# Performance work log

Measured on AMD Instinct MI355X. Metric: run time of the kernel, lower is better.

## Reference

```python
import jax, jax.numpy as jnp
import numpy as np

PI = 3.141592653589793
TAU = 2.0      # tau for both rpe_lif (spikingjelly default 2.0) and act_conv (params['tau'])
V_TH = 1.0     # spikingjelly LIFNode default v_threshold
EPS = 1e-5     # LayerNorm / BatchNorm eps


@jax.custom_vjp
def atan_spike(x):
    # Heaviside forward, ATan surrogate backward (spikingjelly surrogate.ATan, alpha=2)
    return (x >= 0.0).astype(x.dtype)

def _atan_fwd(x):
    return atan_spike(x), x

def _atan_bwd(x, g):
    # (alpha/2) / (1 + ((pi/2)*alpha*x)^2) with alpha=2 -> 1/(1+(pi*x)^2)
    return (g / (1.0 + (PI * x) ** 2),)

atan_spike.defvjp(_atan_fwd, _atan_bwd)


def lif(x_seq, tau=TAU):
    """Multi-step LIF: decay_input=True, v_reset=0, hard reset, detach_reset.
    x_seq: [T, ...]; returns spikes [T, ...]."""
    def step(v, x):
        v = v + (x - v) / tau                      # neuronal charge
        s = atan_spike(v - V_TH)                   # fire
        v = v * (1.0 - jax.lax.stop_gradient(s))   # detached hard reset to 0
        return v, s
    _, spikes = jax.lax.scan(step, jnp.zeros_like(x_seq[0]), x_seq)
    return spikes


def setup_inputs() -> dict:
    key = jax.random.key(0)
    ks = jax.random.split(key, 8)
    B, L, D, T = 256, 50, 128, 4
    n_items, n_h, n_v = 100001, 8, 4
    emb = jax.random.normal(ks[0], (n_items, D), jnp.float32) * 0.5
    emb = emb.at[0].set(0.0)  # padding_idx=0
    return {
        "item_seq": jax.random.randint(ks[1], (B, L), 0, n_items, jnp.int32),
        "emb_table": emb,
        "ln_gamma": jnp.ones((D,), jnp.float32),
        "ln_beta": jnp.zeros((D,), jnp.float32),
        "conv_v_w": jax.random.normal(ks[2], (n_v, L), jnp.float32) * float(1.0 / np.sqrt(L)),
        # per-length kernels stored padded: kernel for length k=i+1 is conv_h_w[i, :, :k, :]
        "conv_h_w": jax.random.normal(ks[3], (L, n_h, L, D), jnp.float32) * 0.02,
        "bn_gamma": jnp.ones((L, n_h), jnp.float32),
        "bn_beta": jnp.zeros((L, n_h), jnp.float32),
        "fc_h_w": jax.random.normal(ks[4], (D, n_h * L), jnp.float32) * 0.05,
        "fc_h_b": jnp.zeros((D,), jnp.float32),
        "fc_v_w": jax.random.normal(ks[5], (D, n_v * D), jnp.float32) * 0.04,
        "fc_v_b": jnp.zeros((D,), jnp.float32),
        "T": 4,
    }


def reference(item_seq, emb_table, ln_gamma, ln_beta, conv_v_w, conv_h_w,
              bn_gamma, bn_beta, fc_h_w, fc_h_b, fc_v_w, fc_v_b, T):
    B, L = item_seq.shape
    D = emb_table.shape[1]
    n_h = conv_h_w.shape[1]
    n_v = conv_v_w.shape[0]

    # embedding + LayerNorm
    emb = emb_table[item_seq]                                   # [B,L,D]
    mu = emb.mean(-1, keepdims=True)
    var = emb.var(-1, keepdims=True)
    x = (emb - mu) / jnp.sqrt(var + EPS) * ln_gamma + ln_beta   # [B,L,D]

    # repeat over T and spike (rpe_lif)
    s = lif(jnp.broadcast_to(x, (T, B, L, D)))                  # binary spikes [T,B,L,D]

    # vertical conv: kernel (L,1), no bias -> collapses seq axis
    out_v = jnp.einsum('tbld,cl->tbcd', s, conv_v_w).reshape(T, B, n_v * D)

    # horizontal multi-scale convs + BN(train stats) + LIF + global max pool
    s2 = s.reshape(T * B, 1, L, D)
    pools = []
    for i in range(L):
        k = i + 1
        w = conv_h_w[i, :, :k, :][:, None]                      # [n_h,1,k,D]
        y = jax.lax.conv_general_dilated(
            s2, w, (1, 1), 'VALID',
            dimension_numbers=('NCHW', 'OIHW', 'NCHW'))[:, :, :, 0]  # [TB,n_h,L-k+1]
        m = y.mean(axis=(0, 2))                                  # BN over (T*B, spatial)
        v = y.var(axis=(0, 2))
        y = (y - m[:, None]) * (bn_gamma[i][:, None] / jnp.sqrt(v[:, None] + EPS)) + bn_beta[i][:, None]
        y = lif(y.reshape(T, B, n_h, L - k + 1))                 # [T,B,n_h,L-k+1]
        pools.append(y.max(axis=-1))                             # [T,B,n_h]
    out_h = jnp.concatenate(pools, axis=-1)                      # [T,B,n_h*L]

    out_h = (out_h @ fc_h_w.T + fc_h_b).mean(0)                  # [B,D]
    out_v = out_v.mean(0) @ fc_v_w.T + fc_v_b                    # [B,D]
    return out_h + out_v
```

## Files before the change

### kernel.cpp

```cpp
#include <hip/hip_runtime.h>

#define B_ 256
#define L_ 50
#define D_ 128
#define T_ 4
#define NH 8
#define NV 4
#define TB_ (T_*B_)
#define EPSF 1e-5f

typedef _Float16 h8 __attribute__((ext_vector_type(8)));
typedef float f4 __attribute__((ext_vector_type(4)));

typedef __attribute__((address_space(1))) const unsigned int gas_u32;
typedef __attribute__((address_space(3))) unsigned int las_u32;
#define GLOAD_LDS16(gp, lp) __builtin_amdgcn_global_load_lds((gas_u32*)(gp), (las_u32*)(lp), 16, 0, 0)

__device__ __forceinline__ float waveSum(float v) {
    #pragma unroll
    for (int o = 32; o > 0; o >>= 1) v += __shfl_down(v, o, 64);
    return v;
}

__device__ __forceinline__ size_t yoff(int i) {
    return (size_t)8192 * (size_t)(50 * i - (i * (i - 1)) / 2);
}

__global__ __launch_bounds__(256) void k0_wsplit(
        const float* __restrict__ w, _Float16* __restrict__ whl) {
    int dk = blockIdx.x, i = blockIdx.y;
    int t = threadIdx.x;
    int c = t >> 4, gd = t & 15;
    int h = c & 7;
    bool live = (i < 50) && (dk <= i);
    const float* src = w + (((size_t)i * NH + h) * L_ + dk) * D_ + gd * 8;
    h8 o;
    #pragma unroll
    for (int e = 0; e < 8; ++e) {
        float wv = live ? src[e] : 0.f;
        _Float16 hi = (_Float16)wv;
        o[e] = (c < 8) ? hi : (_Float16)((wv - (float)hi) * 1024.f);
    }
    *(h8*)(whl + (((size_t)i * 50 + dk) * 16 + c) * 128 + ((gd ^ c) & 15) * 8) = o;
}

__global__ __launch_bounds__(128) void k1_embed_ln_lif(
        const int* __restrict__ item, const float* __restrict__ tab,
        const float* __restrict__ g, const float* __restrict__ be,
        _Float16* __restrict__ s16, float* __restrict__ smean) {
    int bid = blockIdx.x;
    int b = bid / L_, l = bid % L_;
    int d = threadIdx.x;
    int wid = d >> 6, lane = d & 63;
    __shared__ float red[2];
    int it = item[b * L_ + l];
    float e = tab[(size_t)it * D_ + d];
    float sm_ = waveSum(e);
    if (lane == 0) red[wid] = sm_;
    __syncthreads();
    float mu = (red[0] + red[1]) * (1.f / 128.f);
    __syncthreads();
    float df = e - mu;
    float s2 = waveSum(df * df);
    if (lane == 0) red[wid] = s2;
    __syncthreads();
    float var = (red[0] + red[1]) * (1.f / 128.f);
    float x = df / sqrtf(var + EPSF) * g[d] + be[d];
    float v = 0.f, acc = 0.f;
    int pos = (((d >> 3) ^ l) & 15) * 8 + (d & 7);
    #pragma unroll
    for (int t = 0; t < T_; ++t) {
        v += (x - v) * 0.5f;
        float sp = (v >= 1.f) ? 1.f : 0.f;
        v *= (1.f - sp);
        s16[((size_t)(t * B_ + b) * L_ + l) * D_ + pos] = (_Float16)sp;
        acc += sp;
    }
    smean[((size_t)b * L_ + l) * D_ + d] = acc * 0.25f;
}

template<int MTG>
__global__ __launch_bounds__(512, 2) void k2u(
        const _Float16* __restrict__ s16, const _Float16* __restrict__ whl,
        float* __restrict__ y, int gbase) {
    extern __shared__ __align__(16) char lds[];
    char* Bslot = lds + 102400;
    const int NM = 2 * MTG;
    const int tbo = blockIdx.x;
    const int grp = gbase + blockIdx.y;
    const int i0 = grp * 4;
    const int kmax = i0 + 4;
    const int tid = threadIdx.x;
    const int wave = tid >> 6, lane = tid & 63;
    const int p = wave >> 1;
    const int dh = wave & 1;
    const int c_ = lane & 15, g = lane >> 4;

    {
        const float4* src = (const float4*)(s16 + (size_t)tbo * 8 * (L_ * D_));
        float4* dst = (float4*)lds;
        for (int idx = tid; idx < 6400; idx += 512) dst[idx] = src[idx];
    }
    const char* bsrc = (const char*)whl + (size_t)i0 * 50 * 4096;
    const int o0 = tid * 16, o1 = 8192 + tid * 16;
    const int sc0 = o0 >> 12, r0 = o0 & 4095;
    const int sc1 = o1 >> 12, r1 = o1 & 4095;
    const char* g0p = bsrc + (size_t)sc0 * (50 * 4096) + r0;
    const char* g1p = bsrc + (size_t)sc1 * (50 * 4096) + r1;

    float4 n0 = *(const float4*)(g0p);
    float4 n1 = *(const float4*)(g1p);
    __syncthreads();
    *(float4*)(Bslot + o0) = n0;
    *(float4*)(Bslot + o1) = n1;
    __syncthreads();

    f4 acc[4][NM];
    #pragma unroll
    for (int sc = 0; sc < 4; ++sc)
        #pragma unroll
        for (int m = 0; m < NM; ++m) { f4 z = {0.f, 0.f, 0.f, 0.f}; acc[sc][m] = z; }

    for (int dk = 0; dk < kmax; ++dk) {
        const bool more = (dk + 1 < kmax);
        float4 m0, m1;
        if (more) {
            m0 = *(const float4*)(g0p + (size_t)(dk + 1) * 4096);
            m1 = *(const float4*)(g1p + (size_t)(dk + 1) * 4096);
        }
        __builtin_amdgcn_sched_barrier(0);
        #pragma unroll
        for (int dci = 0; dci < 2; ++dci) {
            const int dc = dh * 2 + dci;
            h8 bf[4];
            #pragma unroll
            for (int sc = 0; sc < 4; ++sc)
                bf[sc] = *(const h8*)(Bslot + sc * 4096 + c_ * 256 +
                                      ((((dc << 2) + g) ^ c_) & 15) * 16);
            #pragma unroll
            for (int m = 0; m < NM; ++m) {
                const int tbL = p * 2 + (m >= MTG ? 1 : 0);
                const int jt = (m >= MTG) ? m - MTG : m;
                int l = jt * 16 + c_ + dk; if (l > 49) l = 49;
                h8 a = *(const h8*)(lds + tbL * 12800 + l * 256 +
                                    ((((dc << 2) + g) ^ l) & 15) * 16);
                #pragma unroll
                for (int sc = 0; sc < 4; ++sc)
                    acc[sc][m] = __builtin_amdgcn_mfma_f32_16x16x32_f16(a, bf[sc], acc[sc][m], 0, 0, 0);
            }
        }
        __syncthreads();
        if (more) {
            *(float4*)(Bslot + o0) = m0;
            *(float4*)(Bslot + o1) = m1;
        }
        __syncthreads();
    }

    const int STR = 2 * NM * 4 + 4;
    float* mbuf = (float*)lds;
    #pragma unroll
    for (int half = 0; half < 2; ++half) {
        __syncthreads();
        if (dh == 1) {
            float* wp = mbuf + (size_t)(p * 64 + lane) * STR;
            #pragma unroll
            for (int sc = 0; sc < 2; ++sc)
                #pragma unroll
                for (int m = 0; m < NM; ++m)
                    *(f4*)(wp + (sc * NM + m) * 4) = acc[2 * half + sc][m];
        }
        __syncthreads();
        if (dh == 0) {
            const float* rp = mbuf + (size_t)(p * 64 + lane) * STR;
            #pragma unroll
            for (int sc = 0; sc < 2; ++sc)
                #pragma unroll
                for (int m = 0; m < NM; ++m)
                    acc[2 * half + sc][m] += *(const f4*)(rp + (sc * NM + m) * 4);
        }
    }

    if (dh == 0) {
        const bool hiLane = (c_ < 8);
        const int h = c_ & 7;
        #pragma unroll
        for (int sc = 0; sc < 4; ++sc) {
            const int i = i0 + sc;
            const int J = 50 - i;
            #pragma unroll
            for (int m = 0; m < NM; ++m) {
                const int tbL = p * 2 + (m >= MTG ? 1 : 0);
                const int jt = (m >= MTG) ? m - MTG : m;
                const int tb = tbo * 8 + tbL;
                size_t yb = yoff(i) + ((size_t)tb * NH + h) * J;
                #pragma unroll
                for (int r = 0; r < 4; ++r) {
                    float lo = __shfl_xor(acc[sc][m][r], 8, 64);
                    int j = jt * 16 + g * 4 + r;
                    if (hiLane && j < J) y[yb + j] = acc[sc][m][r] + lo * (1.f / 1024.f);
                }
            }
        }
    }
}

__global__ __launch_bounds__(256, 1) void k2c(
        const _Float16* __restrict__ s16, const _Float16* __restrict__ whl,
        float* __restrict__ y) {
    extern __shared__ __align__(16) char lds[];
    char* bring = lds + 102400;
    const int tbo = blockIdx.x;
    const int i0 = 36 + blockIdx.y * 4;
    const int kmax = (i0 + 4 <= 50) ? (i0 + 4) : 50;
    const int tid = threadIdx.x;
    const int wave = tid >> 6, lane = tid & 63;
    const int tq = wave & 1, sg = wave >> 1;
    const int c_ = lane & 15, g = lane >> 4;

    {
        const float4* src = (const float4*)(s16 + (size_t)tbo * 8 * (L_ * D_));
        float4* dst = (float4*)lds;
        for (int idx = tid; idx < 6400; idx += 256) dst[idx] = src[idx];
    }
    const char* bsrc = (const char*)(whl + ((size_t)(i0 + wave) * 50) * 2048);
    {
        #pragma unroll
        for (int s = 0; s < 2; ++s) {
            const char* gp = bsrc + (size_t)s * 4096 + lane * 16;
            char* lp = bring + s * 16384 + wave * 4096 + lane * 16;
            #pragma unroll
            for (int q = 0; q < 4; ++q)
                GLOAD_LDS16(gp + q * 1024, lp + q * 1024);
        }
    }
    asm volatile("s_waitcnt lgkmcnt(0)" ::: "memory");
    __builtin_amdgcn_s_barrier();
    __builtin_amdgcn_sched_barrier(0);

    f4 acc[2][4];
    #pragma unroll
    for (int s = 0; s < 2; ++s)
        #pragma unroll
        for (int t = 0; t < 4; ++t) { f4 z = {0.f, 0.f, 0.f, 0.f}; acc[s][t] = z; }

    const char* Aq = lds + (tq * 4) * 12800;
    int boff[4];
    #pragma unroll
    for (int dc = 0; dc < 4; ++dc)
        boff[dc] = c_ * 256 + ((((dc << 2) + g) ^ c_) & 15) * 16;

    int rdpos = 0, wrpos = 32768;
    for (int dk = 0; dk < kmax; ++dk) {
        if (dk + 1 < kmax) asm volatile("s_waitcnt vmcnt(4)" ::: "memory");
        else               asm volatile("s_waitcnt vmcnt(0)" ::: "memory");
        __builtin_amdgcn_s_barrier();
        __builtin_amdgcn_sched_barrier(0);
        if (dk + 2 < kmax) {
            const char* gp = bsrc + (size_t)(dk + 2) * 4096 + lane * 16;
            char* lp = bring + wrpos + wave * 4096 + lane * 16;
            #pragma unroll
            for (int q = 0; q < 4; ++q)
                GLOAD_LDS16(gp + q * 1024, lp + q * 1024);
        }
        const char* Bs = bring + rdpos + sg * 8192;
        #pragma unroll
        for (int dc = 0; dc < 4; ++dc) {
            h8 b0 = *(const h8*)(Bs + boff[dc]);
            h8 b1 = *(const h8*)(Bs + 4096 + boff[dc]);
            int l = c_ + dk; if (l > 49) l = 49;
            int aoff = l * 256 + ((((dc << 2) + g) ^ l) & 15) * 16;
            #pragma unroll
            for (int tbL = 0; tbL < 4; ++tbL) {
                h8 a = *(const h8*)(Aq + tbL * 12800 + aoff);
                acc[0][tbL] = __builtin_amdgcn_mfma_f32_16x16x32_f16(a, b0, acc[0][tbL], 0, 0, 0);
                acc[1][tbL] = __builtin_amdgcn_mfma_f32_16x16x32_f16(a, b1, acc[1][tbL], 0, 0, 0);
            }
        }
        rdpos += 16384; if (rdpos == 49152) rdpos = 0;
        wrpos += 16384; if (wrpos == 49152) wrpos = 0;
    }
    const bool hiLane = (c_ < 8);
    const int h = c_ & 7;
    #pragma unroll
    for (int s = 0; s < 2; ++s) {
        const int i = i0 + sg * 2 + s;
        const int J = 50 - i;
        if (J <= 0) continue;
        #pragma unroll
        for (int tbL = 0; tbL < 4; ++tbL) {
            const int tb = tbo * 8 + tq * 4 + tbL;
            size_t yb = yoff(i) + ((size_t)tb * NH + h) * J;
            #pragma unroll
            for (int r = 0; r < 4; ++r) {
                float lo = __shfl_xor(acc[s][tbL][r], 8, 64);
                int j = g * 4 + r;
                if (hiLane && j < J) y[yb + j] = acc[s][tbL][r] + lo * (1.f / 1024.f);
            }
        }
    }
}

__global__ __launch_bounds__(256) void k3_partial(
        const float* __restrict__ y, float* __restrict__ psum) {
    int ih = blockIdx.x, ck = blockIdx.y;
    int i = ih >> 3, h = ih & 7;
    int J = 50 - i;
    size_t yb = yoff(i);
    int tid = threadIdx.x;
    int grp = tid >> 5, sub = tid & 31;
    float sm = 0.f, ss = 0.f;
    for (int tb = ck * 128 + grp; tb < (ck + 1) * 128; tb += 8) {
        const float* row = y + yb + ((size_t)tb * NH + h) * J;
        for (int j = sub; j < J; j += 32) { float v = row[j]; sm += v; ss += v * v; }
    }
    __shared__ float r1[4], r2[4];
    float a = waveSum(sm), b = waveSum(ss);
    int wid = tid >> 6, lane = tid & 63;
    if (lane == 0) { r1[wid] = a; r2[wid] = b; }
    __syncthreads();
    if (tid == 0) {
        psum[((size_t)ih * 8 + ck) * 2]     = r1[0] + r1[1] + r1[2] + r1[3];
        psum[((size_t)ih * 8 + ck) * 2 + 1] = r2[0] + r2[1] + r2[2] + r2[3];
    }
}

__global__ __launch_bounds__(256) void k3_final(
        const float* __restrict__ psum, const float* __restrict__ bng,
        float* __restrict__ statm, float* __restrict__ stats_) {
    int ih = blockIdx.x * 256 + threadIdx.x;
    if (ih >= 400) return;
    float S = 0.f, Q = 0.f;
    for (int ck = 0; ck < 8; ++ck) {
        S += psum[((size_t)ih * 8 + ck) * 2];
        Q += psum[((size_t)ih * 8 + ck) * 2 + 1];
    }
    int i = ih >> 3;
    float cnt = 1024.f * (float)(50 - i);
    float m = S / cnt;
    float var = Q / cnt - m * m; if (var < 0.f) var = 0.f;
    statm[ih] = m;
    stats_[ih] = bng[ih] / sqrtf(var + EPSF);
}

__global__ __launch_bounds__(512) void k4_bn_lif_pool(
        const float* __restrict__ y, const float* __restrict__ statm,
        const float* __restrict__ stats_, const float* __restrict__ bnb,
        float* __restrict__ ps) {
    int b = blockIdx.x, i = blockIdx.y, J = L_ - i;
    int h = threadIdx.x >> 6, lane = threadIdx.x & 63;
    int ih = i * NH + h;
    float m = statm[ih], sc = stats_[ih], bb = bnb[ih];
    size_t yb = yoff(i);
    bool valid = lane < J;
    float v = 0.f; int cnt = 0;
    #pragma unroll
    for (int t = 0; t < T_; ++t) {
        int tb = t * B_ + b;
        float yn;
        if (valid) {
            float raw = y[yb + ((size_t)tb * NH + h) * J + lane];
            yn = (raw - m) * sc + bb;
        } else yn = -1e30f;
        v += (yn - v) * 0.5f;
        bool sp = (v >= 1.f);
        if (sp) v = 0.f;
        if (__any(sp)) cnt++;
    }
    if (lane == 0) ps[(size_t)b * 400 + ih] = (float)cnt;
}

__global__ __launch_bounds__(128) void k5_final(
        const float* __restrict__ smean, const float* __restrict__ ps,
        const float* __restrict__ convv, const float* __restrict__ fchw,
        const float* __restrict__ fchb, const float* __restrict__ fcvw,
        const float* __restrict__ fcvb, float* __restrict__ out) {
    __shared__ float sm_l[L_ * D_];
    __shared__ float vm[NV * D_];
    __shared__ float ps_l[400];
    int b = blockIdx.x, tid = threadIdx.x;
    for (int idx = tid; idx < L_ * D_; idx += 128) sm_l[idx] = smean[(size_t)b * (L_ * D_) + idx];
    for (int idx = tid; idx < 400; idx += 128) ps_l[idx] = ps[(size_t)b * 400 + idx];
    __syncthreads();
    int d = tid;
    #pragma unroll
    for (int c = 0; c < NV; ++c) {
        float a = 0.f;
        for (int l = 0; l < L_; ++l) a += convv[c * L_ + l] * sm_l[l * D_ + d];
        vm[c * D_ + d] = a;
    }
    __syncthreads();
    float acc = fchb[d] + fcvb[d];
    float ah = 0.f;
    for (int ih = 0; ih < 400; ++ih) ah += ps_l[ih] * fchw[d * 400 + ih];
    acc += ah * 0.25f;
    float av = 0.f;
    for (int cd = 0; cd < NV * D_; ++cd) av += vm[cd] * fcvw[d * (NV * D_) + cd];
    acc += av;
    out[(size_t)b * D_ + d] = acc;
}

extern "C" void kernel_launch(void* const* d_in, const int* in_sizes, int n_in,
                              void* d_out, int out_size, void* d_ws, size_t ws_size,
                              hipStream_t stream) {
    const int*   item  = (const int*)d_in[0];
    const float* tab   = (const float*)d_in[1];
    const float* lng   = (const float*)d_in[2];
    const float* lnb   = (const float*)d_in[3];
    const float* convv = (const float*)d_in[4];
    const float* convh = (const float*)d_in[5];
    const float* bng   = (const float*)d_in[6];
    const float* bnb   = (const float*)d_in[7];
    const float* fchw  = (const float*)d_in[8];
    const float* fchb  = (const float*)d_in[9];
    const float* fcvw  = (const float*)d_in[10];
    const float* fcvb  = (const float*)d_in[11];
    float* out = (float*)d_out;

    char* ws = (char*)d_ws;
    _Float16* s16  = (_Float16*)(ws);
    float* smean   = (float*)(ws + 13107200LL);
    float* y       = (float*)(ws + 19660800LL);
    _Float16* whl  = (_Float16*)(ws + 61440000LL);
    float* statm   = (float*)(ws + 72089600LL);
    float* stats_  = (float*)(ws + 72091200LL);
    float* ps      = (float*)(ws + 72092800LL);
    float* psum    = (float*)(ws + 72502400LL);

    hipFuncSetAttribute(reinterpret_cast<const void*>(&k2u<4>),
        hipFuncAttributeMaxDynamicSharedMemorySize, 118784);
    hipFuncSetAttribute(reinterpret_cast<const void*>(&k2u<3>),
        hipFuncAttributeMaxDynamicSharedMemorySize, 118784);
    hipFuncSetAttribute(reinterpret_cast<const void*>(&k2u<2>),
        hipFuncAttributeMaxDynamicSharedMemorySize, 118784);
    hipFuncSetAttribute(reinterpret_cast<const void*>(&k2c),
        hipFuncAttributeMaxDynamicSharedMemorySize, 151552);

    k0_wsplit<<<dim3(50, 52), 256, 0, stream>>>(convh, whl);
    k1_embed_ln_lif<<<B_ * L_, 128, 0, stream>>>(item, tab, lng, lnb, s16, smean);
    k2u<4><<<dim3(128, 1), 512, 118784, stream>>>(s16, whl, y, 0);
    k2u<3><<<dim3(128, 4), 512, 118784, stream>>>(s16, whl, y, 1);
    k2u<2><<<dim3(128, 4), 512, 118784, stream>>>(s16, whl, y, 5);
    k2c<<<dim3(128, 4), 256, 151552, stream>>>(s16, whl, y);
    k3_partial<<<dim3(400, 8), 256, 0, stream>>>(y, psum);
    k3_final<<<dim3(2, 1), 256, 0, stream>>>(psum, bng, statm, stats_);
    k4_bn_lif_pool<<<dim3(B_, L_), 512, 0, stream>>>(y, statm, stats_, bnb, ps);
    k5_final<<<B_, 128, 0, stream>>>(smean, ps, convv, fchw, fchb, fcvw, fcvb, out);
}
```

Measured before the change: 290.6 us.

## Split tail conv kernel across D-chunks with eight waves and LDS reduction

Rewrites the tail multi-scale conv kernel (scales 36-49) to use 512 threads, where each wave owns one D-chunk and all four scales and the partial accumulators are reduced through LDS at the end. The old three-slot async global-to-LDS ring for the weights becomes a register-prefetched single LDS slot with two barriers per step. This lowers LDS to 118784 bytes and gives more waves per block, so the tail kernel gets more parallelism and latency hiding. The costs are extra barriers, a reduction pass, and serialized weight staging.

```diff
diff --git a/kernel.cpp b/kernel.cpp
--- a/kernel.cpp
+++ b/kernel.cpp
@@ -205,97 +205,109 @@
     }
 }
 
-__global__ __launch_bounds__(256, 1) void k2c(
+__global__ __launch_bounds__(512, 2) void k2t(
         const _Float16* __restrict__ s16, const _Float16* __restrict__ whl,
         float* __restrict__ y) {
     extern __shared__ __align__(16) char lds[];
-    char* bring = lds + 102400;
+    char* Bslot = lds + 102400;
     const int tbo = blockIdx.x;
     const int i0 = 36 + blockIdx.y * 4;
     const int kmax = (i0 + 4 <= 50) ? (i0 + 4) : 50;
     const int tid = threadIdx.x;
     const int wave = tid >> 6, lane = tid & 63;
-    const int tq = wave & 1, sg = wave >> 1;
+    const int tq = wave >> 2;
+    const int dc = wave & 3;
     const int c_ = lane & 15, g = lane >> 4;
 
     {
         const float4* src = (const float4*)(s16 + (size_t)tbo * 8 * (L_ * D_));
         float4* dst = (float4*)lds;
-        for (int idx = tid; idx < 6400; idx += 256) dst[idx] = src[idx];
-    }
-    const char* bsrc = (const char*)(whl + ((size_t)(i0 + wave) * 50) * 2048);
-    {
-        #pragma unroll
-        for (int s = 0; s < 2; ++s) {
-            const char* gp = bsrc + (size_t)s * 4096 + lane * 16;
-            char* lp = bring + s * 16384 + wave * 4096 + lane * 16;
-            #pragma unroll
-            for (int q = 0; q < 4; ++q)
-                GLOAD_LDS16(gp + q * 1024, lp + q * 1024);
-        }
-    }
-    asm volatile("s_waitcnt lgkmcnt(0)" ::: "memory");
-    __builtin_amdgcn_s_barrier();
-    __builtin_amdgcn_sched_barrier(0);
-
-    f4 acc[2][4];
-    #pragma unroll
-    for (int s = 0; s < 2; ++s)
-        #pragma unroll
-        for (int t = 0; t < 4; ++t) { f4 z = {0.f, 0.f, 0.f, 0.f}; acc[s][t] = z; }
-
-    const char* Aq = lds + (tq * 4) * 12800;
-    int boff[4];
-    #pragma unroll
-    for (int dc = 0; dc < 4; ++dc)
-        boff[dc] = c_ * 256 + ((((dc << 2) + g) ^ c_) & 15) * 16;
-
-    int rdpos = 0, wrpos = 32768;
+        for (int idx = tid; idx < 6400; idx += 512) dst[idx] = src[idx];
+    }
+    const char* bsrc = (const char*)whl + (size_t)i0 * 50 * 4096;
+    const int o0 = tid * 16, o1 = 8192 + tid * 16;
+    const char* g0p = bsrc + (size_t)(o0 >> 12) * (50 * 4096) + (o0 & 4095);
+    const char* g1p = bsrc + (size_t)(o1 >> 12) * (50 * 4096) + (o1 & 4095);
+    float4 n0 = *(const float4*)(g0p);
+    float4 n1 = *(const float4*)(g1p);
+    __syncthreads();
+    *(float4*)(Bslot + o0) = n0;
+    *(float4*)(Bslot + o1) = n1;
+    __syncthreads();
+
+    f4 acc[4][4];
+    #pragma unroll
+    for (int sc = 0; sc < 4; ++sc)
+        #pragma unroll
+        for (int tt = 0; tt < 4; ++tt) { f4 z = {0.f, 0.f, 0.f, 0.f}; acc[sc][tt] = z; }
+
+    const int boffc = c_ * 256 + ((((dc << 2) + g) ^ c_) & 15) * 16;
     for (int dk = 0; dk < kmax; ++dk) {
-        if (dk + 1 < kmax) asm volatile("s_waitcnt vmcnt(4)" ::: "memory");
-        else               asm volatile("s_waitcnt vmcnt(0)" ::: "memory");
-        __builtin_amdgcn_s_barrier();
+        const bool more = (dk + 1 < kmax);
+        float4 m0, m1;
+        if (more) {
+            m0 = *(const float4*)(g0p + (size_t)(dk + 1) * 4096);
+            m1 = *(const float4*)(g1p + (size_t)(dk + 1) * 4096);
+        }
         __builtin_amdgcn_sched_barrier(0);
-        if (dk + 2 < kmax) {
-            const char* gp = bsrc + (size_t)(dk + 2) * 4096 + lane * 16;
-            char* lp = bring + wrpos + wave * 4096 + lane * 16;
-            #pragma unroll
-            for (int q = 0; q < 4; ++q)
-                GLOAD_LDS16(gp + q * 1024, lp + q * 1024);
-        }
-        const char* Bs = bring + rdpos + sg * 8192;
-        #pragma unroll
-        for (int dc = 0; dc < 4; ++dc) {
-            h8 b0 = *(const h8*)(Bs + boff[dc]);
-            h8 b1 = *(const h8*)(Bs + 4096 + boff[dc]);
-            int l = c_ + dk; if (l > 49) l = 49;
-            int aoff = l * 256 + ((((dc << 2) + g) ^ l) & 15) * 16;
-            #pragma unroll
-            for (int tbL = 0; tbL < 4; ++tbL) {
-                h8 a = *(const h8*)(Aq + tbL * 12800 + aoff);
-                acc[0][tbL] = __builtin_amdgcn_mfma_f32_16x16x32_f16(a, b0, acc[0][tbL], 0, 0, 0);
-                acc[1][tbL] = __builtin_amdgcn_mfma_f32_16x16x32_f16(a, b1, acc[1][tbL], 0, 0, 0);
-            }
-        }
-        rdpos += 16384; if (rdpos == 49152) rdpos = 0;
-        wrpos += 16384; if (wrpos == 49152) wrpos = 0;
-    }
-    const bool hiLane = (c_ < 8);
-    const int h = c_ & 7;
-    #pragma unroll
-    for (int s = 0; s < 2; ++s) {
-        const int i = i0 + sg * 2 + s;
-        const int J = 50 - i;
-        if (J <= 0) continue;
-        #pragma unroll
-        for (int tbL = 0; tbL < 4; ++tbL) {
-            const int tb = tbo * 8 + tq * 4 + tbL;
-            size_t yb = yoff(i) + ((size_t)tb * NH + h) * J;
-            #pragma unroll
-            for (int r = 0; r < 4; ++r) {
-                float lo = __shfl_xor(acc[s][tbL][r], 8, 64);
-                int j = g * 4 + r;
-                if (hiLane && j < J) y[yb + j] = acc[s][tbL][r] + lo * (1.f / 1024.f);
+        h8 bf[4];
+        #pragma unroll
+        for (int sc = 0; sc < 4; ++sc)
+            bf[sc] = *(const h8*)(Bslot + sc * 4096 + boffc);
+        int l = c_ + dk; if (l > 49) l = 49;
+        const int aoff = l * 256 + ((((dc << 2) + g) ^ l) & 15) * 16;
+        #pragma unroll
+        for (int tt = 0; tt < 4; ++tt) {
+            h8 a = *(const h8*)(lds + (tq * 4 + tt) * 12800 + aoff);
+            #pragma unroll
+            for (int sc = 0; sc < 4; ++sc)
+                acc[sc][tt] = __builtin_amdgcn_mfma_f32_16x16x32_f16(a, bf[sc], acc[sc][tt], 0, 0, 0);
+        }
+        __syncthreads();
+        if (more) {
+            *(float4*)(Bslot + o0) = m0;
+            *(float4*)(Bslot + o1) = m1;
+        }
+        __syncthreads();
+    }
+
+    f4* mbuf = (f4*)lds;
+    if (dc != 0) {
+        f4* wp = mbuf + (size_t)(((dc - 1) * 2 + tq) * 16) * 64 + lane;
+        #pragma unroll
+        for (int sc = 0; sc < 4; ++sc)
+            #pragma unroll
+            for (int tt = 0; tt < 4; ++tt)
+                wp[(sc * 4 + tt) * 64] = acc[sc][tt];
+    }
+    __syncthreads();
+    if (dc == 0) {
+        #pragma unroll
+        for (int dd = 0; dd < 3; ++dd) {
+            const f4* rp = mbuf + (size_t)((dd * 2 + tq) * 16) * 64 + lane;
+            #pragma unroll
+            for (int sc = 0; sc < 4; ++sc)
+                #pragma unroll
+                for (int tt = 0; tt < 4; ++tt)
+                    acc[sc][tt] += rp[(sc * 4 + tt) * 64];
+        }
+        const bool hiLane = (c_ < 8);
+        const int h = c_ & 7;
+        #pragma unroll
+        for (int sc = 0; sc < 4; ++sc) {
+            const int i = i0 + sc;
+            const int J = 50 - i;
+            if (J <= 0) continue;
+            #pragma unroll
+            for (int tt = 0; tt < 4; ++tt) {
+                const int tb = tbo * 8 + tq * 4 + tt;
+                size_t yb = yoff(i) + ((size_t)tb * NH + h) * J;
+                #pragma unroll
+                for (int r = 0; r < 4; ++r) {
+                    float lo = __shfl_xor(acc[sc][tt][r], 8, 64);
+                    int j = g * 4 + r;
+                    if (hiLane && j < J) y[yb + j] = acc[sc][tt][r] + lo * (1.f / 1024.f);
+                }
             }
         }
     }
@@ -433,15 +445,15 @@
         hipFuncAttributeMaxDynamicSharedMemorySize, 118784);
     hipFuncSetAttribute(reinterpret_cast<const void*>(&k2u<2>),
         hipFuncAttributeMaxDynamicSharedMemorySize, 118784);
-    hipFuncSetAttribute(reinterpret_cast<const void*>(&k2c),
-        hipFuncAttributeMaxDynamicSharedMemorySize, 151552);
+    hipFuncSetAttribute(reinterpret_cast<const void*>(&k2t),
+        hipFuncAttributeMaxDynamicSharedMemorySize, 118784);
 
     k0_wsplit<<<dim3(50, 52), 256, 0, stream>>>(convh, whl);
     k1_embed_ln_lif<<<B_ * L_, 128, 0, stream>>>(item, tab, lng, lnb, s16, smean);
     k2u<4><<<dim3(128, 1), 512, 118784, stream>>>(s16, whl, y, 0);
     k2u<3><<<dim3(128, 4), 512, 118784, stream>>>(s16, whl, y, 1);
     k2u<2><<<dim3(128, 4), 512, 118784, stream>>>(s16, whl, y, 5);
-    k2c<<<dim3(128, 4), 256, 151552, stream>>>(s16, whl, y);
+    k2t<<<dim3(128, 4), 512, 118784, stream>>>(s16, whl, y);
     k3_partial<<<dim3(400, 8), 256, 0, stream>>>(y, psum);
     k3_final<<<dim3(2, 1), 256, 0, stream>>>(psum, bng, statm, stats_);
     k4_bn_lif_pool<<<dim3(B_, L_), 512, 0, stream>>>(y, statm, stats_, bnb, ps);
```

Result: faster. 281.7 us (-3.0%).
